# Kernel optimization log

Hardware: AMD Instinct MI355X
Metric: run time of the kernel (lower is better)

## Reference

```python
import jax, jax.numpy as jnp
import numpy as np

B, S, L, C = 256, 3, 4096, 2        # batch, num_slices, slice_length, in_channels
NN, CH, GH, HEADS = 4, 64, 64, 4    # num_nodes, cnn_hidden, gat_hidden, gat_heads
BD = CH * NN // 2                   # CNN branch_dim = 128
TD, TH, TL = 256, 4, 2              # transformer dim / heads / layers
NC = 5
DH = TD // TH


def setup_inputs():
    ks = iter(jax.random.split(jax.random.key(0), 128))
    def rn(shape, s=0.05):
        return jax.random.normal(next(ks), shape, jnp.float32) * s
    def bn(c):  # eval-mode BN params: gamma, beta, running_mean, running_var
        return (jax.random.uniform(next(ks), (2, c)) + 0.5, rn((2, c)),
                rn((2, c)), jax.random.uniform(next(ks), (2, c)) + 0.5)
    inp = {}
    inp['x_t'] = jax.random.normal(next(ks), (B, S, L, C), jnp.float32)
    inp['x_f'] = jax.random.uniform(next(ks), (B, S, L, C), jnp.float32)
    # dual-branch CNN params stacked on leading axis: [0]=time branch, [1]=freq branch
    inp['conv1_w'] = rn((2, 32, C, 15)); inp['conv1_b'] = rn((2, 32))
    inp['bn1_g'], inp['bn1_b'], inp['bn1_m'], inp['bn1_v'] = bn(32)
    inp['conv2_w'] = rn((2, 64, 32, 7)); inp['conv2_b'] = rn((2, 64))
    inp['bn2_g'], inp['bn2_b'], inp['bn2_m'], inp['bn2_v'] = bn(64)
    inp['conv3_w'] = rn((2, BD, 64, 3)); inp['conv3_b'] = rn((2, BD))
    inp['bn3_g'], inp['bn3_b'], inp['bn3_m'], inp['bn3_v'] = bn(BD)
    # PyG GATConv params (lin has no bias; att_src/att_dst per head; output bias)
    inp['gat_lin_w'] = rn((HEADS * GH, CH))
    inp['gat_att_src'] = rn((HEADS, GH)); inp['gat_att_dst'] = rn((HEADS, GH))
    inp['gat_bias'] = rn((HEADS * GH,))
    inp['feat_proj_w'] = rn((TD, NN * GH * HEADS)); inp['feat_proj_b'] = rn((TD,))
    # TransformerEncoder (post-norm, relu), params stacked over TL layers
    inp['tr_in_w'] = rn((TL, 3 * TD, TD)); inp['tr_in_b'] = rn((TL, 3 * TD))
    inp['tr_out_w'] = rn((TL, TD, TD)); inp['tr_out_b'] = rn((TL, TD))
    inp['tr_l1_w'] = rn((TL, 4 * TD, TD)); inp['tr_l1_b'] = rn((TL, 4 * TD))
    inp['tr_l2_w'] = rn((TL, TD, 4 * TD)); inp['tr_l2_b'] = rn((TL, TD))
    inp['tr_ln1_g'] = jnp.ones((TL, TD)); inp['tr_ln1_b'] = jnp.zeros((TL, TD))
    inp['tr_ln2_g'] = jnp.ones((TL, TD)); inp['tr_ln2_b'] = jnp.zeros((TL, TD))
    inp['ta_w'] = rn((1, TD)); inp['ta_b'] = rn((1,))
    inp['fc1_w'] = rn((128, TD)); inp['fc1_b'] = rn((128,))
    inp['fc2_w'] = rn((64, 128)); inp['fc2_b'] = rn((64,))
    inp['fc3_w'] = rn((NC, 64)); inp['fc3_b'] = rn((NC,))
    src = [i for i in range(NN) for j in range(NN) if i != j]
    dst = [j for i in range(NN) for j in range(NN) if i != j]
    inp['edge_index'] = jnp.array([src, dst], jnp.int32)
    return inp


def _conv_bn_relu(x, w, b, g, be, m, v, stride, pad):
    y = jax.lax.conv_general_dilated(x, w, (stride,), [(pad, pad)],
                                     dimension_numbers=('NCH', 'OIH', 'NCH'))
    y = (y + b[None, :, None] - m[None, :, None]) * (g / jnp.sqrt(v + 1e-5))[None, :, None] + be[None, :, None]
    return jax.nn.relu(y)


def _branch(x, c1w, c1b, g1, b1, m1, v1, c2w, c2b, g2, b2, m2, v2, c3w, c3b, g3, b3, m3, v3):
    y = _conv_bn_relu(x, c1w, c1b, g1, b1, m1, v1, 2, 7)
    y = _conv_bn_relu(y, c2w, c2b, g2, b2, m2, v2, 2, 3)
    y = _conv_bn_relu(y, c3w, c3b, g3, b3, m3, v3, 1, 1)
    return y.mean(axis=-1)  # AdaptiveAvgPool1d(1)


def _ln(x, g, b):
    mu = x.mean(-1, keepdims=True)
    var = ((x - mu) ** 2).mean(-1, keepdims=True)
    return (x - mu) / jnp.sqrt(var + 1e-5) * g + b


def _model(edge_index, x_t, x_f, conv1_w, conv1_b, bn1_g, bn1_b, bn1_m, bn1_v,
           conv2_w, conv2_b, bn2_g, bn2_b, bn2_m, bn2_v,
           conv3_w, conv3_b, bn3_g, bn3_b, bn3_m, bn3_v,
           gat_lin_w, gat_att_src, gat_att_dst, gat_bias,
           feat_proj_w, feat_proj_b,
           tr_in_w, tr_in_b, tr_out_w, tr_out_b, tr_l1_w, tr_l1_b, tr_l2_w, tr_l2_b,
           tr_ln1_g, tr_ln1_b, tr_ln2_g, tr_ln2_b,
           ta_w, ta_b, fc1_w, fc1_b, fc2_w, fc2_b, fc3_w, fc3_b):
    G = B * S  # fold (batch, slice) -> one big conv/GAT batch (replaces the python loops)
    xt = x_t.transpose(0, 1, 3, 2).reshape(G, C, L)
    xf = x_f.transpose(0, 1, 3, 2).reshape(G, C, L)
    xs = jnp.stack([xt, xf])  # [2, G, C, L]
    pooled = jax.vmap(_branch)(xs, conv1_w, conv1_b, bn1_g, bn1_b, bn1_m, bn1_v,
                               conv2_w, conv2_b, bn2_g, bn2_b, bn2_m, bn2_v,
                               conv3_w, conv3_b, bn3_g, bn3_b, bn3_m, bn3_v)  # [2, G, BD]
    feat = jnp.concatenate([pooled[0], pooled[1]], axis=1).reshape(G, NN, CH)
    # GATConv (dense over the tiny 4-node graph; softmax over in-edges per dest node)
    h = jnp.einsum('gnc,oc->gno', feat, gat_lin_w).reshape(G, NN, HEADS, GH)
    a_src = jnp.einsum('gnhd,hd->gnh', h, gat_att_src)
    a_dst = jnp.einsum('gnhd,hd->gnh', h, gat_att_dst)
    scores = jax.nn.leaky_relu(a_dst[:, :, None, :] + a_src[:, None, :, :], 0.2)  # [G,i,j,H]
    adj = jnp.zeros((NN, NN), bool).at[edge_index[1], edge_index[0]].set(True)
    adj = adj.at[jnp.arange(NN), jnp.arange(NN)].set(True)  # PyG adds self-loops
    alpha = jax.nn.softmax(jnp.where(adj[None, :, :, None], scores, -1e9), axis=2)
    gat_out = jnp.einsum('gijh,gjhd->gihd', alpha, h).reshape(G, NN, HEADS * GH) + gat_bias
    sl = gat_out.reshape(B, S, NN * HEADS * GH) @ feat_proj_w.T + feat_proj_b  # [B,S,TD]
    # positional encoding
    pos = jnp.arange(S, dtype=jnp.float32)[:, None]
    div = jnp.exp(jnp.arange(0, TD, 2, dtype=jnp.float32) * (-np.log(10000.0) / TD))
    pe = jnp.zeros((S, TD)).at[:, 0::2].set(jnp.sin(pos * div)).at[:, 1::2].set(jnp.cos(pos * div))
    x = sl + pe[None]
    # TransformerEncoder, post-norm, relu FFN
    for l in range(TL):
        qkv = x @ tr_in_w[l].T + tr_in_b[l]
        q, k, v = jnp.split(qkv, 3, axis=-1)
        q = q.reshape(B, S, TH, DH).transpose(0, 2, 1, 3)
        k = k.reshape(B, S, TH, DH).transpose(0, 2, 1, 3)
        v = v.reshape(B, S, TH, DH).transpose(0, 2, 1, 3)
        attn = jax.nn.softmax(jnp.einsum('bhqd,bhkd->bhqk', q, k) / np.sqrt(DH), axis=-1)
        a = jnp.einsum('bhqk,bhkd->bhqd', attn, v).transpose(0, 2, 1, 3).reshape(B, S, TD)
        a = a @ tr_out_w[l].T + tr_out_b[l]
        x = _ln(x + a, tr_ln1_g[l], tr_ln1_b[l])
        f = jax.nn.relu(x @ tr_l1_w[l].T + tr_l1_b[l]) @ tr_l2_w[l].T + tr_l2_b[l]
        x = _ln(x + f, tr_ln2_g[l], tr_ln2_b[l])
    w = jax.nn.softmax((x @ ta_w.T + ta_b)[..., 0], axis=1)  # [B,S] temporal attention
    ctx = jnp.einsum('bs,bsd->bd', w, x)
    o = jax.nn.relu(ctx @ fc1_w.T + fc1_b)
    o = jax.nn.relu(o @ fc2_w.T + fc2_b)
    return o @ fc3_w.T + fc3_b  # logits [B, NC]


def reference(x_t, x_f, conv1_w, conv1_b, bn1_g, bn1_b, bn1_m, bn1_v, conv2_w, conv2_b, bn2_g, bn2_b, bn2_m, bn2_v, conv3_w, conv3_b, bn3_g, bn3_b, bn3_m, bn3_v, gat_lin_w, gat_att_src, gat_att_dst, gat_bias, feat_proj_w, feat_proj_b, tr_in_w, tr_in_b, tr_out_w, tr_out_b, tr_l1_w, tr_l1_b, tr_l2_w, tr_l2_b, tr_ln1_g, tr_ln1_b, tr_ln2_g, tr_ln2_b, ta_w, ta_b, fc1_w, fc1_b, fc2_w, fc2_b, fc3_w, fc3_b, edge_index):
    return _model(edge_index, x_t, x_f, conv1_w, conv1_b, bn1_g, bn1_b, bn1_m, bn1_v,
                  conv2_w, conv2_b, bn2_g, bn2_b, bn2_m, bn2_v,
                  conv3_w, conv3_b, bn3_g, bn3_b, bn3_m, bn3_v,
                  gat_lin_w, gat_att_src, gat_att_dst, gat_bias,
                  feat_proj_w, feat_proj_b,
                  tr_in_w, tr_in_b, tr_out_w, tr_out_b, tr_l1_w, tr_l1_b, tr_l2_w, tr_l2_b,
                  tr_ln1_g, tr_ln1_b, tr_ln2_g, tr_ln2_b,
                  ta_w, ta_b, fc1_w, fc1_b, fc2_w, fc2_b, fc3_w, fc3_b)
```

## Files before the change

### kernel.cpp

```cpp
#include <hip/hip_runtime.h>
#include <math.h>

#define Bn 256
#define Sn 3
#define Ln 4096
#define Gn 768
#define TDn 256
#define TLn 2

#define WS_W1K   0
#define WS_W2K   1024
#define WS_W3K   15360
#define WS_H1    39936
#define WS_H2    40000
#define WS_H3    40128
#define WS_FPWH  40960
#define WS_INWH  172032
#define WS_OUTWH 368640
#define WS_L1WH  434176
#define WS_L2WH  696320
#define WS_POOL  958464
#define WS_XH    958464
#define WS_ABH   1056768
#define WS_SCR   1155072
#define WS_Y     1548288
#define WS_X     1744896

typedef _Float16 f16x8 __attribute__((ext_vector_type(8)));
typedef float f32x4 __attribute__((ext_vector_type(4)));
#define MFMA16(a,b,c) __builtin_amdgcn_mfma_f32_16x16x32_f16(a,b,c,0,0,0)

__global__ __launch_bounds__(256) void prep_kernel(
    const float* __restrict__ w1, const float* __restrict__ w2, const float* __restrict__ w3,
    const float* __restrict__ c1b, const float* __restrict__ g1, const float* __restrict__ b1,
    const float* __restrict__ m1, const float* __restrict__ v1,
    const float* __restrict__ c2b, const float* __restrict__ g2, const float* __restrict__ b2,
    const float* __restrict__ m2, const float* __restrict__ v2,
    const float* __restrict__ c3b, const float* __restrict__ g3, const float* __restrict__ b3,
    const float* __restrict__ m3, const float* __restrict__ v3,
    float* __restrict__ ws)
{
    int i = blockIdx.x * 256 + threadIdx.x;
    _Float16* w1k = (_Float16*)(ws + WS_W1K);
    _Float16* w2k = (_Float16*)(ws + WS_W2K);
    _Float16* w3k = (_Float16*)(ws + WS_W3K);
    if (i < 2048) {
        int k = i & 31, oc = (i >> 5) & 31, br = i >> 10;
        int c = k >> 4, tau = k & 15;
        int a = br * 32 + oc;
        float s = g1[a] / sqrtf(v1[a] + 1e-5f);
        float v = (tau < 15) ? w1[(((size_t)a * 2 + c) * 15) + tau] * s : 0.f;
        w1k[i] = (_Float16)v;
    }
    if (i < 28672) {
        int k = i % 224; int a = i / 224;
        int tblk = k >> 5, ic = k & 31;
        int t = (tblk < 4) ? 2 * tblk : 2 * (tblk - 4) + 1;
        float s = g2[a] / sqrtf(v2[a] + 1e-5f);
        w2k[i] = (_Float16)(w2[((size_t)a * 32 + ic) * 7 + t] * s);
    }
    if (i < 49152) {
        int k = i % 192; int a = i / 192;
        int t = k >> 6, ic = k & 63;
        float s = g3[a] / sqrtf(v3[a] + 1e-5f);
        w3k[i] = (_Float16)(w3[((size_t)a * 64 + ic) * 3 + t] * s);
    }
    if (i < 64)  { float s = g1[i] / sqrtf(v1[i] + 1e-5f); ws[WS_H1 + i] = (c1b[i] - m1[i]) * s + b1[i]; }
    if (i < 128) { float s = g2[i] / sqrtf(v2[i] + 1e-5f); ws[WS_H2 + i] = (c2b[i] - m2[i]) * s + b2[i]; }
    if (i < 256) { float s = g3[i] / sqrtf(v3[i] + 1e-5f); ws[WS_H3 + i] = (c3b[i] - m3[i]) * s + b3[i]; }
}

__global__ __launch_bounds__(256) void prep_tr_kernel(
    const float* __restrict__ fpw, const float* __restrict__ inw,
    const float* __restrict__ outw, const float* __restrict__ l1w,
    const float* __restrict__ l2w, float* __restrict__ ws)
{
    int i = blockIdx.x * 256 + threadIdx.x;
    _Float16* fpwh = (_Float16*)(ws + WS_FPWH);
    _Float16* inwh = (_Float16*)(ws + WS_INWH);
    _Float16* outwh = (_Float16*)(ws + WS_OUTWH);
    _Float16* l1wh = (_Float16*)(ws + WS_L1WH);
    _Float16* l2wh = (_Float16*)(ws + WS_L2WH);
    if (i < 262144) fpwh[i] = (_Float16)fpw[i];
    if (i < 393216) inwh[i] = (_Float16)inw[i];
    if (i < 131072) outwh[i] = (_Float16)outw[i];
    if (i < 524288) { l1wh[i] = (_Float16)l1w[i]; l2wh[i] = (_Float16)l2w[i]; }
}

__global__ __launch_bounds__(256, 3) void conv_mfma_kernel(
    const float* __restrict__ x_t, const float* __restrict__ x_f,
    const float* __restrict__ ws, float* __restrict__ pooled)
{
    __shared__ _Float16 xsf[2 * 576];
    __shared__ _Float16 y1[2][132 * 32];
    __shared__ _Float16 y2s[128 * 64];
    __shared__ float h1s[32];
    __shared__ float h2s[64];
    __shared__ float h3s[128];
    __shared__ float pbuf[128];

    const int g = blockIdx.x, br = blockIdx.y;
    const int tid = threadIdx.x;
    const int lane = tid & 63, wv = tid >> 6;
    const int l15 = lane & 15, q4 = lane >> 4;

    const float* xin = (br == 0 ? x_t : x_f) + (size_t)g * (Ln * 2);
    const _Float16* w1k = (const _Float16*)(ws + WS_W1K) + br * 1024;
    const _Float16* w2k = (const _Float16*)(ws + WS_W2K) + br * 14336;
    const _Float16* w3k = (const _Float16*)(ws + WS_W3K) + br * 24576;

    if (tid < 32)  h1s[tid] = ws[WS_H1 + br * 32 + tid];
    if (tid < 64)  h2s[tid] = ws[WS_H2 + br * 64 + tid];
    if (tid < 128) { h3s[tid] = ws[WS_H3 + br * 128 + tid]; pbuf[tid] = 0.f; }

    f16x8 a1[2];
    #pragma unroll
    for (int mt = 0; mt < 2; ++mt)
        a1[mt] = *(const f16x8*)(w1k + (mt * 16 + l15) * 32 + q4 * 8);

    const int mg = wv & 1, ng = wv >> 1;

    const _Float16* w2row = w2k + (size_t)l15 * 224 + q4 * 8;
    const _Float16* w3row = w3k + (size_t)(mg * 64 + l15) * 192 + q4 * 8;

    float pool_[4][4];
    #pragma unroll
    for (int mt = 0; mt < 4; ++mt)
        #pragma unroll
        for (int r = 0; r < 4; ++r) pool_[mt][r] = 0.f;

    const f32x4 vzero = {0.f, 0.f, 0.f, 0.f};

    for (int l = tid; l < 576; l += 256) {
        int xl = -17 + l;
        float a = 0.f, b = 0.f;
        if (xl >= 0 && xl < Ln) { float2 v = *(const float2*)(xin + (size_t)xl * 2); a = v.x; b = v.y; }
        xsf[l] = (_Float16)a; xsf[576 + l] = (_Float16)b;
    }
    __syncthreads();

    #pragma unroll 1
    for (int tile = 0; tile < 9; ++tile) {
        const int P0 = tile * 126;
        const int Q0 = 2 * P0 - 5;

        const uint* xsu = (const uint*)xsf;
        #pragma unroll 1
        for (int nt = wv; nt < 17; nt += 4) {
            int j0 = nt * 16 + l15;
            union { f16x8 v; uint u[4]; } bf;
            int ubase = (q4 >> 1) * 288 + j0 + (q4 & 1) * 4;
            #pragma unroll
            for (int ii = 0; ii < 4; ++ii) bf.u[ii] = xsu[ubase + ii];
            f32x4 c1acc[2] = {vzero, vzero};
            c1acc[0] = MFMA16(a1[0], bf.v, c1acc[0]);
            c1acc[1] = MFMA16(a1[1], bf.v, c1acc[1]);

            if (j0 <= 260) {
                int q = Q0 + j0;
                bool val = (q >= 0) && (q < 2048);
                int i = j0 >> 1, par = j0 & 1;
                #pragma unroll
                for (int mt = 0; mt < 2; ++mt) {
                    int oc0 = mt * 16 + q4 * 4;
                    union { _Float16 h[4]; uint2 u; } pk;
                    #pragma unroll
                    for (int r = 0; r < 4; ++r) {
                        float y = c1acc[mt][r] + h1s[oc0 + r];
                        y = y > 0.f ? y : 0.f;
                        pk.h[r] = val ? (_Float16)y : (_Float16)0.f;
                    }
                    int gq = mt * 2 + (q4 >> 1), sub = q4 & 1;
                    *(uint2*)(&y1[par][(i * 4 + (gq ^ (i & 3))) * 8 + sub * 4]) = pk.u;
                }
            }
        }
        __syncthreads();

        float2 xr0 = {0.f, 0.f}, xr1 = {0.f, 0.f}, xr2 = {0.f, 0.f};
        if (tile < 8) {
            const int xn0 = 4 * (P0 + 126) - 17;
            { int xl = xn0 + tid;       if (xl < Ln) xr0 = *(const float2*)(xin + (size_t)xl * 2); }
            { int xl = xn0 + tid + 256; if (xl < Ln) xr1 = *(const float2*)(xin + (size_t)xl * 2); }
            if (tid < 64) { int xl = xn0 + tid + 512; if (xl < Ln) xr2 = *(const float2*)(xin + (size_t)xl * 2); }
        }

        #pragma unroll 1
        for (int jj = 0; jj < 2; ++jj) {
            f32x4 c2[4] = {vzero, vzero, vzero, vzero};
            f16x8 a2c[4];
            #pragma unroll
            for (int mt = 0; mt < 4; ++mt)
                a2c[mt] = *(const f16x8*)(w2row + (size_t)mt * 16 * 224);
            const int n = wv * 32 + jj * 16 + l15;
            #pragma unroll 1
            for (int ks = 0; ks < 7; ++ks) {
                int roff = (ks < 4) ? ks : ks - 4;
                const _Float16* yb = y1[(ks < 4) ? 0 : 1];
                int i = n + roff;
                f16x8 bb = *(const f16x8*)(yb + (i * 4 + (q4 ^ (i & 3))) * 8);
                f16x8 a2n[4];
                if (ks < 6) {
                    #pragma unroll
                    for (int mt = 0; mt < 4; ++mt)
                        a2n[mt] = *(const f16x8*)(w2row + (size_t)mt * 16 * 224 + (ks + 1) * 32);
                }
                #pragma unroll
                for (int mt = 0; mt < 4; ++mt)
                    c2[mt] = MFMA16(a2c[mt], bb, c2[mt]);
                if (ks < 6) {
                    #pragma unroll
                    for (int mt = 0; mt < 4; ++mt) a2c[mt] = a2n[mt];
                }
            }
            int p2 = P0 - 1 + n;
            bool val = (p2 >= 0) && (p2 < 1024);
            #pragma unroll
            for (int mt = 0; mt < 4; ++mt) {
                int oc0 = mt * 16 + q4 * 4;
                union { _Float16 h[4]; uint2 u; } pk;
                #pragma unroll
                for (int r = 0; r < 4; ++r) {
                    float y = c2[mt][r] + h2s[oc0 + r];
                    y = y > 0.f ? y : 0.f;
                    pk.h[r] = val ? (_Float16)y : (_Float16)0.f;
                }
                int gq = oc0 >> 3, sub = q4 & 1;
                *(uint2*)(&y2s[(n * 8 + (gq ^ (n & 7))) * 8 + sub * 4]) = pk.u;
            }
        }

        if (tile < 8) {
            { int l = tid;       xsf[l] = (_Float16)xr0.x; xsf[576 + l] = (_Float16)xr0.y; }
            { int l = tid + 256; xsf[l] = (_Float16)xr1.x; xsf[576 + l] = (_Float16)xr1.y; }
            if (tid < 64) { int l = tid + 512; xsf[l] = (_Float16)xr2.x; xsf[576 + l] = (_Float16)xr2.y; }
        }
        __syncthreads();

        #pragma unroll 1
        for (int half = 0; half < 2; ++half) {
            f32x4 c3[4][2];
            #pragma unroll
            for (int mt = 0; mt < 4; ++mt) { c3[mt][0] = vzero; c3[mt][1] = vzero; }
            f16x8 a3c[4];
            #pragma unroll
            for (int mt = 0; mt < 4; ++mt)
                a3c[mt] = *(const f16x8*)(w3row + (size_t)mt * 16 * 192);
            #pragma unroll 1
            for (int ks = 0; ks < 6; ++ks) {
                int t = ks >> 1, ich = ks & 1;
                f16x8 b3[2];
                #pragma unroll
                for (int jj = 0; jj < 2; ++jj) {
                    int np = ng * 64 + (half * 2 + jj) * 16 + l15;
                    int r = np + t; r = r < 128 ? r : 127;
                    int gq3 = ich * 4 + q4;
                    b3[jj] = *(const f16x8*)(&y2s[(r * 8 + (gq3 ^ (r & 7))) * 8]);
                }
                f16x8 a3n[4];
                if (ks < 5) {
                    #pragma unroll
                    for (int mt = 0; mt < 4; ++mt)
                        a3n[mt] = *(const f16x8*)(w3row + (size_t)mt * 16 * 192 + (ks + 1) * 32);
                }
                #pragma unroll
                for (int mt = 0; mt < 4; ++mt) {
                    c3[mt][0] = MFMA16(a3c[mt], b3[0], c3[mt][0]);
                    c3[mt][1] = MFMA16(a3c[mt], b3[1], c3[mt][1]);
                }
                if (ks < 5) {
                    #pragma unroll
                    for (int mt = 0; mt < 4; ++mt) a3c[mt] = a3n[mt];
                }
            }
            #pragma unroll
            for (int mt = 0; mt < 4; ++mt) {
                int oc0 = mg * 64 + mt * 16 + q4 * 4;
                #pragma unroll
                for (int jj = 0; jj < 2; ++jj) {
                    int np = ng * 64 + (half * 2 + jj) * 16 + l15;
                    int p3 = P0 + np;
                    float valf = ((np < 126) && (p3 < 1024)) ? 1.f : 0.f;
                    #pragma unroll
                    for (int r = 0; r < 4; ++r) {
                        float y = c3[mt][jj][r] + h3s[oc0 + r];
                        y = y > 0.f ? y : 0.f;
                        pool_[mt][r] = fmaf(y, valf, pool_[mt][r]);
                    }
                }
            }
        }
    }

    #pragma unroll
    for (int mt = 0; mt < 4; ++mt)
        #pragma unroll
        for (int r = 0; r < 4; ++r) {
            float v = pool_[mt][r];
            v += __shfl_xor(v, 1, 64);
            v += __shfl_xor(v, 2, 64);
            v += __shfl_xor(v, 4, 64);
            v += __shfl_xor(v, 8, 64);
            if (l15 == 0) atomicAdd(&pbuf[mg * 64 + mt * 16 + q4 * 4 + r], v);
        }
    __syncthreads();
    if (tid < 128) pooled[g * 256 + br * 128 + tid] = pbuf[tid] * (1.f / 1024.f);
}

__global__ __launch_bounds__(256) void gat_kernel(
    const float* __restrict__ glw, const float* __restrict__ att_src,
    const float* __restrict__ att_dst, const float* __restrict__ gbias,
    const float* __restrict__ pooled, _Float16* __restrict__ gouth)
{
    __shared__ float feats[256];
    __shared__ float hs[4 * 256];
    __shared__ float av[32];
    __shared__ float alpha[64];

    int g = blockIdx.x, tid = threadIdx.x;
    feats[tid] = pooled[g * 256 + tid];
    __syncthreads();

    {
        int o = tid;
        const float* w = glw + o * 64;
        float a0 = 0, a1 = 0, a2 = 0, a3 = 0;
        for (int c = 0; c < 64; ++c) {
            float wvv = w[c];
            a0 = fmaf(feats[c],       wvv, a0);
            a1 = fmaf(feats[64 + c],  wvv, a1);
            a2 = fmaf(feats[128 + c], wvv, a2);
            a3 = fmaf(feats[192 + c], wvv, a3);
        }
        hs[o] = a0; hs[256 + o] = a1; hs[512 + o] = a2; hs[768 + o] = a3;
    }
    __syncthreads();

    if (tid < 32) {
        int n = (tid & 15) >> 2, hd = tid & 3;
        const float* aw = (tid < 16) ? att_src : att_dst;
        float s = 0;
        for (int d = 0; d < 64; ++d) s = fmaf(hs[n * 256 + hd * 64 + d], aw[hd * 64 + d], s);
        av[tid] = s;
    }
    __syncthreads();

    if (tid < 16) {
        int i = tid >> 2, hd = tid & 3;
        float sc[4], mx = -1e30f;
        #pragma unroll
        for (int j = 0; j < 4; ++j) {
            float v = av[16 + i * 4 + hd] + av[j * 4 + hd];
            v = v > 0.f ? v : 0.2f * v;
            sc[j] = v; mx = fmaxf(mx, v);
        }
        float den = 0;
        #pragma unroll
        for (int j = 0; j < 4; ++j) { sc[j] = expf(sc[j] - mx); den += sc[j]; }
        #pragma unroll
        for (int j = 0; j < 4; ++j) alpha[(i * 4 + j) * 4 + hd] = sc[j] / den;
    }
    __syncthreads();

    {
        int o = tid, hd = o >> 6;
        #pragma unroll
        for (int i = 0; i < 4; ++i) {
            float acc = gbias[o];
            #pragma unroll
            for (int j = 0; j < 4; ++j) acc = fmaf(alpha[(i * 4 + j) * 4 + hd], hs[j * 256 + o], acc);
            gouth[(size_t)g * 1024 + i * 256 + o] = (_Float16)acc;
        }
    }
}

template <int K, int MODE>
__global__ __launch_bounds__(256) void mfma_gemm_kernel(
    const _Float16* __restrict__ A, const _Float16* __restrict__ W,
    const float* __restrict__ bias, float* __restrict__ out32,
    _Float16* __restrict__ out16, int N)
{
    const int tid = threadIdx.x;
    const int wv = tid >> 6, l15 = tid & 15, q4 = (tid & 63) >> 4;
    const int m0 = blockIdx.x * 64 + wv * 16;
    const int n0 = blockIdx.y * 64;

    const f32x4 vzero = {0.f, 0.f, 0.f, 0.f};
    f32x4 acc[4] = {vzero, vzero, vzero, vzero};

    const _Float16* arow = A + (size_t)(m0 + l15) * K + q4 * 8;
    #pragma unroll 4
    for (int ks = 0; ks < K / 32; ++ks) {
        f16x8 a = *(const f16x8*)(arow + ks * 32);
        #pragma unroll
        for (int nt = 0; nt < 4; ++nt) {
            f16x8 b = *(const f16x8*)(W + (size_t)(n0 + nt * 16 + l15) * K + ks * 32 + q4 * 8);
            acc[nt] = MFMA16(a, b, acc[nt]);
        }
    }

    #pragma unroll
    for (int nt = 0; nt < 4; ++nt) {
        int n = n0 + nt * 16 + l15;
        float bs = bias[n];
        #pragma unroll
        for (int r = 0; r < 4; ++r) {
            int m = m0 + q4 * 4 + r;
            float v = acc[nt][r] + bs;
            if (MODE == 1) v = fmaxf(v, 0.f);
            if (MODE == 3) {
                int s = m % 3;
                int kk = n >> 1;
                float dv = expf((float)kk * -0.07195588f);
                float arg = (float)s * dv;
                v += (n & 1) ? cosf(arg) : sinf(arg);
            }
            if (MODE == 0 || MODE == 3) out32[(size_t)m * N + n] = v;
            if (MODE == 1 || MODE == 3) out16[(size_t)m * N + n] = (_Float16)v;
        }
    }
}

template <int K>
__global__ __launch_bounds__(256) void gemm_ln_kernel(
    const _Float16* __restrict__ A, const _Float16* __restrict__ W,
    const float* __restrict__ bias,
    const float* __restrict__ gamma, const float* __restrict__ beta,
    float* __restrict__ X, _Float16* __restrict__ XH)
{
    __shared__ float ys[16][260];
    const int tid = threadIdx.x;
    const int wv = tid >> 6, l15 = tid & 15, q4 = (tid & 63) >> 4;
    const int r0 = blockIdx.x * 16;
    const int n0 = wv * 64;

    const f32x4 vzero = {0.f, 0.f, 0.f, 0.f};
    f32x4 acc[4] = {vzero, vzero, vzero, vzero};

    const _Float16* arow = A + (size_t)(r0 + l15) * K + q4 * 8;
    #pragma unroll 4
    for (int ks = 0; ks < K / 32; ++ks) {
        f16x8 a = *(const f16x8*)(arow + ks * 32);
        #pragma unroll
        for (int nt = 0; nt < 4; ++nt) {
            f16x8 b = *(const f16x8*)(W + (size_t)(n0 + nt * 16 + l15) * K + ks * 32 + q4 * 8);
            acc[nt] = MFMA16(a, b, acc[nt]);
        }
    }

    #pragma unroll
    for (int nt = 0; nt < 4; ++nt) {
        int col = n0 + nt * 16 + l15;
        float bs = bias[col];
        #pragma unroll
        for (int r = 0; r < 4; ++r) {
            int rowl = q4 * 4 + r;
            ys[rowl][col] = acc[nt][r] + bs + X[(size_t)(r0 + rowl) * 256 + col];
        }
    }
    __syncthreads();

    {
        int row = tid >> 4, l16 = tid & 15;
        float s = 0, s2 = 0;
        #pragma unroll
        for (int c0 = 0; c0 < 256; c0 += 16) {
            float v = ys[row][c0 + l16]; s += v; s2 += v * v;
        }
        s += __shfl_xor(s, 1, 64);  s2 += __shfl_xor(s2, 1, 64);
        s += __shfl_xor(s, 2, 64);  s2 += __shfl_xor(s2, 2, 64);
        s += __shfl_xor(s, 4, 64);  s2 += __shfl_xor(s2, 4, 64);
        s += __shfl_xor(s, 8, 64);  s2 += __shfl_xor(s2, 8, 64);
        float mu = s * (1.f / 256.f);
        float var = s2 * (1.f / 256.f) - mu * mu;
        float inv = 1.0f / sqrtf(var + 1e-5f);
        #pragma unroll
        for (int c0 = 0; c0 < 256; c0 += 16) {
            int c = c0 + l16;
            float v = (ys[row][c] - mu) * inv * gamma[c] + beta[c];
            X[(size_t)(r0 + row) * 256 + c] = v;
            XH[(size_t)(r0 + row) * 256 + c] = (_Float16)v;
        }
    }
}

__global__ __launch_bounds__(256) void attn_kernel(
    const float* __restrict__ qkv, _Float16* __restrict__ abufh)
{
    int b = blockIdx.x, tid = threadIdx.x, head = tid >> 6, d = tid & 63;
    const float* base = qkv + (size_t)b * 3 * 768 + head * 64 + d;
    float q[3], k[3], v[3];
    #pragma unroll
    for (int s = 0; s < 3; ++s) {
        const float* row = base + s * 768;
        q[s] = row[0]; k[s] = row[256]; v[s] = row[512];
    }
    float sc[3][3];
    #pragma unroll
    for (int si = 0; si < 3; ++si)
        #pragma unroll
        for (int sj = 0; sj < 3; ++sj) {
            float p = q[si] * k[sj];
            #pragma unroll
            for (int m = 32; m > 0; m >>= 1) p += __shfl_xor(p, m, 64);
            sc[si][sj] = p * 0.125f;
        }
    #pragma unroll
    for (int si = 0; si < 3; ++si) {
        float mx = fmaxf(sc[si][0], fmaxf(sc[si][1], sc[si][2]));
        float e0 = expf(sc[si][0] - mx), e1 = expf(sc[si][1] - mx), e2 = expf(sc[si][2] - mx);
        float den = e0 + e1 + e2;
        float o = (e0 * v[0] + e1 * v[1] + e2 * v[2]) / den;
        abufh[(size_t)(b * 3 + si) * 256 + head * 64 + d] = (_Float16)o;
    }
}

__global__ __launch_bounds__(256) void head_kernel(
    const float* __restrict__ X, const float* __restrict__ taw, const float* __restrict__ tab,
    const float* __restrict__ f1w, const float* __restrict__ f1b,
    const float* __restrict__ f2w, const float* __restrict__ f2b,
    const float* __restrict__ f3w, const float* __restrict__ f3b,
    float* __restrict__ out)
{
    __shared__ float xs[3 * 256];
    __shared__ float wsm[3];
    __shared__ float cs[256];
    __shared__ float a1[128];
    __shared__ float a2[64];
    int b = blockIdx.x, tid = threadIdx.x;
    for (int idx = tid; idx < 768; idx += 256) xs[idx] = X[(size_t)b * 768 + idx];
    __syncthreads();
    if (tid < 3) {
        float s = tab[0];
        for (int d = 0; d < 256; ++d) s = fmaf(xs[tid * 256 + d], taw[d], s);
        wsm[tid] = s;
    }
    __syncthreads();
    {
        float m = fmaxf(wsm[0], fmaxf(wsm[1], wsm[2]));
        float e0 = expf(wsm[0] - m), e1 = expf(wsm[1] - m), e2 = expf(wsm[2] - m);
        float den = e0 + e1 + e2;
        cs[tid] = (e0 * xs[tid] + e1 * xs[256 + tid] + e2 * xs[512 + tid]) / den;
    }
    __syncthreads();
    if (tid < 128) {
        float a = f1b[tid];
        const float* w = f1w + tid * 256;
        for (int c = 0; c < 256; ++c) a = fmaf(cs[c], w[c], a);
        a1[tid] = fmaxf(a, 0.f);
    }
    __syncthreads();
    if (tid < 64) {
        float a = f2b[tid];
        const float* w = f2w + tid * 128;
        for (int c = 0; c < 128; ++c) a = fmaf(a1[c], w[c], a);
        a2[tid] = fmaxf(a, 0.f);
    }
    __syncthreads();
    if (tid < 5) {
        float a = f3b[tid];
        const float* w = f3w + tid * 64;
        for (int c = 0; c < 64; ++c) a = fmaf(a2[c], w[c], a);
        out[b * 5 + tid] = a;
    }
}

extern "C" void kernel_launch(void* const* d_in, const int* in_sizes, int n_in,
                              void* d_out, int out_size, void* d_ws, size_t ws_size,
                              hipStream_t stream) {
    const float* x_t     = (const float*)d_in[0];
    const float* x_f     = (const float*)d_in[1];
    const float* conv1_w = (const float*)d_in[2];
    const float* conv1_b = (const float*)d_in[3];
    const float* bn1_g   = (const float*)d_in[4];
    const float* bn1_b   = (const float*)d_in[5];
    const float* bn1_m   = (const float*)d_in[6];
    const float* bn1_v   = (const float*)d_in[7];
    const float* conv2_w = (const float*)d_in[8];
    const float* conv2_b = (const float*)d_in[9];
    const float* bn2_g   = (const float*)d_in[10];
    const float* bn2_b   = (const float*)d_in[11];
    const float* bn2_m   = (const float*)d_in[12];
    const float* bn2_v   = (const float*)d_in[13];
    const float* conv3_w = (const float*)d_in[14];
    const float* conv3_b = (const float*)d_in[15];
    const float* bn3_g   = (const float*)d_in[16];
    const float* bn3_b   = (const float*)d_in[17];
    const float* bn3_m   = (const float*)d_in[18];
    const float* bn3_v   = (const float*)d_in[19];
    const float* gat_lin_w   = (const float*)d_in[20];
    const float* gat_att_src = (const float*)d_in[21];
    const float* gat_att_dst = (const float*)d_in[22];
    const float* gat_bias    = (const float*)d_in[23];
    const float* feat_proj_w = (const float*)d_in[24];
    const float* feat_proj_b = (const float*)d_in[25];
    const float* tr_in_w  = (const float*)d_in[26];
    const float* tr_in_b  = (const float*)d_in[27];
    const float* tr_out_w = (const float*)d_in[28];
    const float* tr_out_b = (const float*)d_in[29];
    const float* tr_l1_w  = (const float*)d_in[30];
    const float* tr_l1_b  = (const float*)d_in[31];
    const float* tr_l2_w  = (const float*)d_in[32];
    const float* tr_l2_b  = (const float*)d_in[33];
    const float* tr_ln1_g = (const float*)d_in[34];
    const float* tr_ln1_b = (const float*)d_in[35];
    const float* tr_ln2_g = (const float*)d_in[36];
    const float* tr_ln2_b = (const float*)d_in[37];
    const float* ta_w  = (const float*)d_in[38];
    const float* ta_b  = (const float*)d_in[39];
    const float* fc1_w = (const float*)d_in[40];
    const float* fc1_b = (const float*)d_in[41];
    const float* fc2_w = (const float*)d_in[42];
    const float* fc2_b = (const float*)d_in[43];
    const float* fc3_w = (const float*)d_in[44];
    const float* fc3_b = (const float*)d_in[45];

    float* ws    = (float*)d_ws;
    float* POOL  = ws + WS_POOL;
    float* X     = ws + WS_X;
    float* QKV   = ws + WS_SCR;
    _Float16* GOUTH = (_Float16*)(ws + WS_SCR);
    _Float16* MIDH  = (_Float16*)(ws + WS_SCR);
    _Float16* XH    = (_Float16*)(ws + WS_XH);
    _Float16* ABH   = (_Float16*)(ws + WS_ABH);
    const _Float16* FPWH  = (const _Float16*)(ws + WS_FPWH);
    const _Float16* INWH  = (const _Float16*)(ws + WS_INWH);
    const _Float16* OUTWH = (const _Float16*)(ws + WS_OUTWH);
    const _Float16* L1WH  = (const _Float16*)(ws + WS_L1WH);
    const _Float16* L2WH  = (const _Float16*)(ws + WS_L2WH);
    float* out = (float*)d_out;

    prep_kernel<<<192, 256, 0, stream>>>(conv1_w, conv2_w, conv3_w,
        conv1_b, bn1_g, bn1_b, bn1_m, bn1_v,
        conv2_b, bn2_g, bn2_b, bn2_m, bn2_v,
        conv3_b, bn3_g, bn3_b, bn3_m, bn3_v, ws);
    prep_tr_kernel<<<2048, 256, 0, stream>>>(feat_proj_w, tr_in_w, tr_out_w,
                                             tr_l1_w, tr_l2_w, ws);

    conv_mfma_kernel<<<dim3(Gn, 2), 256, 0, stream>>>(x_t, x_f, ws, POOL);

    gat_kernel<<<Gn, 256, 0, stream>>>(gat_lin_w, gat_att_src, gat_att_dst, gat_bias,
                                       POOL, GOUTH);

    mfma_gemm_kernel<1024, 3><<<dim3(12, 4), 256, 0, stream>>>(
        GOUTH, FPWH, feat_proj_b, X, XH, 256);

    for (int l = 0; l < TLn; ++l) {
        mfma_gemm_kernel<256, 0><<<dim3(12, 12), 256, 0, stream>>>(
            XH, INWH + (size_t)l * 196608, tr_in_b + l * 768, QKV, nullptr, 768);
        attn_kernel<<<Bn, 256, 0, stream>>>(QKV, ABH);
        gemm_ln_kernel<256><<<48, 256, 0, stream>>>(
            ABH, OUTWH + (size_t)l * 65536, tr_out_b + l * 256,
            tr_ln1_g + l * 256, tr_ln1_b + l * 256, X, XH);
        mfma_gemm_kernel<256, 1><<<dim3(12, 16), 256, 0, stream>>>(
            XH, L1WH + (size_t)l * 262144, tr_l1_b + l * 1024, nullptr, MIDH, 1024);
        gemm_ln_kernel<1024><<<48, 256, 0, stream>>>(
            MIDH, L2WH + (size_t)l * 262144, tr_l2_b + l * 256,
            tr_ln2_g + l * 256, tr_ln2_b + l * 256, X, XH);
    }

    head_kernel<<<Bn, 256, 0, stream>>>(X, ta_w, ta_b, fc1_w, fc1_b,
                                        fc2_w, fc2_b, fc3_w, fc3_b, out);
}
```

Before: 764.8 us.

## Fuse transformer layer into attention and FFN kernels; restructure conv2 MFMA loop

The per-layer chain of QKV GEMM, attention, out-proj+LN, FFN1 and FFN2+LN, five launches, becomes two fused kernels. One kernel per batch computes QKV, attention, out-projection and LayerNorm in shared memory. The other runs FFN1 and FFN2 with LayerNorm over 16-row tiles, keeping the intermediate in LDS. This removes launch overhead and global round-trips of the QKV and MLP intermediates. The attention kernel uses only 3 of 16 MFMA rows, wasting matrix throughput, and the FFN kernel launches only 48 blocks. Separately, the conv2 stage now computes both column halves per weight load, and conv occupancy is lowered from 3 to 2 to make room for the extra registers.

```diff
diff --git a/kernel.cpp b/kernel.cpp
--- a/kernel.cpp
+++ b/kernel.cpp
@@ -21,9 +21,7 @@
 #define WS_L2WH  696320
 #define WS_POOL  958464
 #define WS_XH    958464
-#define WS_ABH   1056768
 #define WS_SCR   1155072
-#define WS_Y     1548288
 #define WS_X     1744896
 
 typedef _Float16 f16x8 __attribute__((ext_vector_type(8)));
@@ -87,7 +85,7 @@
     if (i < 524288) { l1wh[i] = (_Float16)l1w[i]; l2wh[i] = (_Float16)l2w[i]; }
 }
 
-__global__ __launch_bounds__(256, 3) void conv_mfma_kernel(
+__global__ __launch_bounds__(256, 2) void conv_mfma_kernel(
     const float* __restrict__ x_t, const float* __restrict__ x_f,
     const float* __restrict__ ws, float* __restrict__ pooled)
 {
@@ -185,20 +183,25 @@
             if (tid < 64) { int xl = xn0 + tid + 512; if (xl < Ln) xr2 = *(const float2*)(xin + (size_t)xl * 2); }
         }
 
-        #pragma unroll 1
-        for (int jj = 0; jj < 2; ++jj) {
-            f32x4 c2[4] = {vzero, vzero, vzero, vzero};
+        {
+            f32x4 c2[4][2];
+            #pragma unroll
+            for (int mt = 0; mt < 4; ++mt) { c2[mt][0] = vzero; c2[mt][1] = vzero; }
             f16x8 a2c[4];
             #pragma unroll
             for (int mt = 0; mt < 4; ++mt)
                 a2c[mt] = *(const f16x8*)(w2row + (size_t)mt * 16 * 224);
-            const int n = wv * 32 + jj * 16 + l15;
             #pragma unroll 1
             for (int ks = 0; ks < 7; ++ks) {
                 int roff = (ks < 4) ? ks : ks - 4;
                 const _Float16* yb = y1[(ks < 4) ? 0 : 1];
-                int i = n + roff;
-                f16x8 bb = *(const f16x8*)(yb + (i * 4 + (q4 ^ (i & 3))) * 8);
+                f16x8 bb[2];
+                #pragma unroll
+                for (int jj = 0; jj < 2; ++jj) {
+                    int n = wv * 32 + jj * 16 + l15;
+                    int i = n + roff;
+                    bb[jj] = *(const f16x8*)(yb + (i * 4 + (q4 ^ (i & 3))) * 8);
+                }
                 f16x8 a2n[4];
                 if (ks < 6) {
                     #pragma unroll
@@ -206,27 +209,33 @@
                         a2n[mt] = *(const f16x8*)(w2row + (size_t)mt * 16 * 224 + (ks + 1) * 32);
                 }
                 #pragma unroll
-                for (int mt = 0; mt < 4; ++mt)
-                    c2[mt] = MFMA16(a2c[mt], bb, c2[mt]);
+                for (int mt = 0; mt < 4; ++mt) {
+                    c2[mt][0] = MFMA16(a2c[mt], bb[0], c2[mt][0]);
+                    c2[mt][1] = MFMA16(a2c[mt], bb[1], c2[mt][1]);
+                }
                 if (ks < 6) {
                     #pragma unroll
                     for (int mt = 0; mt < 4; ++mt) a2c[mt] = a2n[mt];
                 }
             }
-            int p2 = P0 - 1 + n;
-            bool val = (p2 >= 0) && (p2 < 1024);
-            #pragma unroll
-            for (int mt = 0; mt < 4; ++mt) {
-                int oc0 = mt * 16 + q4 * 4;
-                union { _Float16 h[4]; uint2 u; } pk;
-                #pragma unroll
-                for (int r = 0; r < 4; ++r) {
-                    float y = c2[mt][r] + h2s[oc0 + r];
-                    y = y > 0.f ? y : 0.f;
-                    pk.h[r] = val ? (_Float16)y : (_Float16)0.f;
-                }
-                int gq = oc0 >> 3, sub = q4 & 1;
-                *(uint2*)(&y2s[(n * 8 + (gq ^ (n & 7))) * 8 + sub * 4]) = pk.u;
+            #pragma unroll
+            for (int jj = 0; jj < 2; ++jj) {
+                int n = wv * 32 + jj * 16 + l15;
+                int p2 = P0 - 1 + n;
+                bool val = (p2 >= 0) && (p2 < 1024);
+                #pragma unroll
+                for (int mt = 0; mt < 4; ++mt) {
+                    int oc0 = mt * 16 + q4 * 4;
+                    union { _Float16 h[4]; uint2 u; } pk;
+                    #pragma unroll
+                    for (int r = 0; r < 4; ++r) {
+                        float y = c2[mt][jj][r] + h2s[oc0 + r];
+                        y = y > 0.f ? y : 0.f;
+                        pk.h[r] = val ? (_Float16)y : (_Float16)0.f;
+                    }
+                    int gq = oc0 >> 3, sub = q4 & 1;
+                    *(uint2*)(&y2s[(n * 8 + (gq ^ (n & 7))) * 8 + sub * 4]) = pk.u;
+                }
             }
         }
 
@@ -374,16 +383,16 @@
     }
 }
 
-template <int K, int MODE>
-__global__ __launch_bounds__(256) void mfma_gemm_kernel(
+__global__ __launch_bounds__(256) void fproj_gemm_kernel(
     const _Float16* __restrict__ A, const _Float16* __restrict__ W,
     const float* __restrict__ bias, float* __restrict__ out32,
-    _Float16* __restrict__ out16, int N)
+    _Float16* __restrict__ out16)
 {
     const int tid = threadIdx.x;
     const int wv = tid >> 6, l15 = tid & 15, q4 = (tid & 63) >> 4;
     const int m0 = blockIdx.x * 64 + wv * 16;
     const int n0 = blockIdx.y * 64;
+    constexpr int K = 1024;
 
     const f32x4 vzero = {0.f, 0.f, 0.f, 0.f};
     f32x4 acc[4] = {vzero, vzero, vzero, vzero};
@@ -403,66 +412,206 @@
     for (int nt = 0; nt < 4; ++nt) {
         int n = n0 + nt * 16 + l15;
         float bs = bias[n];
+        int kk = n >> 1;
+        float dv = expf((float)kk * -0.07195588f);
         #pragma unroll
         for (int r = 0; r < 4; ++r) {
             int m = m0 + q4 * 4 + r;
             float v = acc[nt][r] + bs;
-            if (MODE == 1) v = fmaxf(v, 0.f);
-            if (MODE == 3) {
-                int s = m % 3;
-                int kk = n >> 1;
-                float dv = expf((float)kk * -0.07195588f);
-                float arg = (float)s * dv;
-                v += (n & 1) ? cosf(arg) : sinf(arg);
-            }
-            if (MODE == 0 || MODE == 3) out32[(size_t)m * N + n] = v;
-            if (MODE == 1 || MODE == 3) out16[(size_t)m * N + n] = (_Float16)v;
-        }
-    }
-}
-
-template <int K>
-__global__ __launch_bounds__(256) void gemm_ln_kernel(
-    const _Float16* __restrict__ A, const _Float16* __restrict__ W,
-    const float* __restrict__ bias,
-    const float* __restrict__ gamma, const float* __restrict__ beta,
-    float* __restrict__ X, _Float16* __restrict__ XH)
+            float arg = (float)(m % 3) * dv;
+            v += (n & 1) ? cosf(arg) : sinf(arg);
+            out32[(size_t)m * 256 + n] = v;
+            out16[(size_t)m * 256 + n] = (_Float16)v;
+        }
+    }
+}
+
+__global__ __launch_bounds__(256) void attn_fused_kernel(
+    _Float16* __restrict__ XH, float* __restrict__ X,
+    const _Float16* __restrict__ inw, const float* __restrict__ inb,
+    const _Float16* __restrict__ outw, const float* __restrict__ outb,
+    const float* __restrict__ gamma, const float* __restrict__ beta)
 {
+    __shared__ _Float16 xls[3 * 264];
+    __shared__ float qkvl[3 * 768];
+    __shared__ _Float16 aout[3 * 264];
+    __shared__ float ys[3][256];
+
+    const int b = blockIdx.x, tid = threadIdx.x;
+    const int wv = tid >> 6, lane = tid & 63;
+    const int l15 = tid & 15, q4 = (tid & 63) >> 4;
+    const int ml = (l15 < 3) ? l15 : 2;
+
+    for (int idx = tid; idx < 768; idx += 256)
+        xls[(idx >> 8) * 264 + (idx & 255)] = XH[(size_t)b * 768 + idx];
+    __syncthreads();
+
+    {
+        const int n0w = wv * 192;
+        const _Float16* arow = xls + ml * 264 + q4 * 8;
+        #pragma unroll 1
+        for (int nt = 0; nt < 12; ++nt) {
+            int col = n0w + nt * 16 + l15;
+            f32x4 acc = {0.f, 0.f, 0.f, 0.f};
+            #pragma unroll
+            for (int ks = 0; ks < 8; ++ks) {
+                f16x8 a = *(const f16x8*)(arow + ks * 32);
+                f16x8 bf = *(const f16x8*)(inw + (size_t)col * 256 + ks * 32 + q4 * 8);
+                acc = MFMA16(a, bf, acc);
+            }
+            if (q4 == 0) {
+                float bsv = inb[col];
+                #pragma unroll
+                for (int r = 0; r < 3; ++r)
+                    qkvl[r * 768 + col] = acc[r] + bsv;
+            }
+        }
+    }
+    __syncthreads();
+
+    {
+        const int hb = wv * 64 + lane;
+        float q[3], k[3], v[3];
+        #pragma unroll
+        for (int s = 0; s < 3; ++s) {
+            q[s] = qkvl[s * 768 + hb];
+            k[s] = qkvl[s * 768 + 256 + hb];
+            v[s] = qkvl[s * 768 + 512 + hb];
+        }
+        float sc[3][3];
+        #pragma unroll
+        for (int si = 0; si < 3; ++si)
+            #pragma unroll
+            for (int sj = 0; sj < 3; ++sj) {
+                float p = q[si] * k[sj];
+                #pragma unroll
+                for (int m = 32; m > 0; m >>= 1) p += __shfl_xor(p, m, 64);
+                sc[si][sj] = p * 0.125f;
+            }
+        #pragma unroll
+        for (int si = 0; si < 3; ++si) {
+            float mx = fmaxf(sc[si][0], fmaxf(sc[si][1], sc[si][2]));
+            float e0 = expf(sc[si][0] - mx), e1 = expf(sc[si][1] - mx), e2 = expf(sc[si][2] - mx);
+            float den = e0 + e1 + e2;
+            float o = (e0 * v[0] + e1 * v[1] + e2 * v[2]) / den;
+            aout[si * 264 + hb] = (_Float16)o;
+        }
+    }
+    __syncthreads();
+
+    {
+        const int n0w = wv * 64;
+        const _Float16* arow = aout + ml * 264 + q4 * 8;
+        #pragma unroll 1
+        for (int nt = 0; nt < 4; ++nt) {
+            int col = n0w + nt * 16 + l15;
+            f32x4 acc = {0.f, 0.f, 0.f, 0.f};
+            #pragma unroll
+            for (int ks = 0; ks < 8; ++ks) {
+                f16x8 a = *(const f16x8*)(arow + ks * 32);
+                f16x8 bf = *(const f16x8*)(outw + (size_t)col * 256 + ks * 32 + q4 * 8);
+                acc = MFMA16(a, bf, acc);
+            }
+            if (q4 == 0) {
+                float bsv = outb[col];
+                #pragma unroll
+                for (int r = 0; r < 3; ++r)
+                    ys[r][col] = acc[r] + bsv + X[((size_t)b * 3 + r) * 256 + col];
+            }
+        }
+    }
+    __syncthreads();
+
+    if (wv < 3) {
+        float s = 0.f, s2 = 0.f;
+        #pragma unroll
+        for (int c0 = 0; c0 < 256; c0 += 64) {
+            float v = ys[wv][c0 + lane]; s += v; s2 += v * v;
+        }
+        #pragma unroll
+        for (int m = 32; m > 0; m >>= 1) { s += __shfl_xor(s, m, 64); s2 += __shfl_xor(s2, m, 64); }
+        float mu = s * (1.f / 256.f);
+        float var = s2 * (1.f / 256.f) - mu * mu;
+        float inv = 1.f / sqrtf(var + 1e-5f);
+        #pragma unroll
+        for (int c0 = 0; c0 < 256; c0 += 64) {
+            int c = c0 + lane;
+            float v = (ys[wv][c] - mu) * inv * gamma[c] + beta[c];
+            X[((size_t)b * 3 + wv) * 256 + c] = v;
+            XH[((size_t)b * 3 + wv) * 256 + c] = (_Float16)v;
+        }
+    }
+}
+
+__global__ __launch_bounds__(256) void ffn_fused_kernel(
+    _Float16* __restrict__ XH, float* __restrict__ X,
+    const _Float16* __restrict__ l1w, const float* __restrict__ l1b,
+    const _Float16* __restrict__ l2w, const float* __restrict__ l2b,
+    const float* __restrict__ gamma, const float* __restrict__ beta)
+{
+    __shared__ _Float16 xls[16 * 264];
+    __shared__ _Float16 mid[16 * 1032];
     __shared__ float ys[16][260];
+
     const int tid = threadIdx.x;
     const int wv = tid >> 6, l15 = tid & 15, q4 = (tid & 63) >> 4;
     const int r0 = blockIdx.x * 16;
-    const int n0 = wv * 64;
-
-    const f32x4 vzero = {0.f, 0.f, 0.f, 0.f};
-    f32x4 acc[4] = {vzero, vzero, vzero, vzero};
-
-    const _Float16* arow = A + (size_t)(r0 + l15) * K + q4 * 8;
-    #pragma unroll 4
-    for (int ks = 0; ks < K / 32; ++ks) {
-        f16x8 a = *(const f16x8*)(arow + ks * 32);
+
+    for (int idx = tid; idx < 4096; idx += 256)
+        xls[(idx >> 8) * 264 + (idx & 255)] = XH[(size_t)r0 * 256 + idx];
+    __syncthreads();
+
+    {
+        const _Float16* arow = xls + l15 * 264 + q4 * 8;
+        #pragma unroll 1
+        for (int nt = 0; nt < 16; ++nt) {
+            int col = wv * 256 + nt * 16 + l15;
+            f32x4 acc = {0.f, 0.f, 0.f, 0.f};
+            #pragma unroll
+            for (int ks = 0; ks < 8; ++ks) {
+                f16x8 a = *(const f16x8*)(arow + ks * 32);
+                f16x8 bf = *(const f16x8*)(l1w + (size_t)col * 256 + ks * 32 + q4 * 8);
+                acc = MFMA16(a, bf, acc);
+            }
+            float bsv = l1b[col];
+            #pragma unroll
+            for (int r = 0; r < 4; ++r) {
+                float v = fmaxf(acc[r] + bsv, 0.f);
+                mid[(q4 * 4 + r) * 1032 + col] = (_Float16)v;
+            }
+        }
+    }
+    __syncthreads();
+
+    {
+        const _Float16* arow = mid + l15 * 1032 + q4 * 8;
+        const f32x4 vzero = {0.f, 0.f, 0.f, 0.f};
+        f32x4 acc[4] = {vzero, vzero, vzero, vzero};
+        #pragma unroll 2
+        for (int ks = 0; ks < 32; ++ks) {
+            f16x8 a = *(const f16x8*)(arow + ks * 32);
+            #pragma unroll
+            for (int nt = 0; nt < 4; ++nt) {
+                f16x8 bf = *(const f16x8*)(l2w + (size_t)(wv * 64 + nt * 16 + l15) * 1024 + ks * 32 + q4 * 8);
+                acc[nt] = MFMA16(a, bf, acc[nt]);
+            }
+        }
         #pragma unroll
         for (int nt = 0; nt < 4; ++nt) {
-            f16x8 b = *(const f16x8*)(W + (size_t)(n0 + nt * 16 + l15) * K + ks * 32 + q4 * 8);
-            acc[nt] = MFMA16(a, b, acc[nt]);
-        }
-    }
-
-    #pragma unroll
-    for (int nt = 0; nt < 4; ++nt) {
-        int col = n0 + nt * 16 + l15;
-        float bs = bias[col];
-        #pragma unroll
-        for (int r = 0; r < 4; ++r) {
-            int rowl = q4 * 4 + r;
-            ys[rowl][col] = acc[nt][r] + bs + X[(size_t)(r0 + rowl) * 256 + col];
+            int col = wv * 64 + nt * 16 + l15;
+            float bsv = l2b[col];
+            #pragma unroll
+            for (int r = 0; r < 4; ++r) {
+                int row = q4 * 4 + r;
+                ys[row][col] = acc[nt][r] + bsv + X[(size_t)(r0 + row) * 256 + col];
+            }
         }
     }
     __syncthreads();
 
     {
         int row = tid >> 4, l16 = tid & 15;
-        float s = 0, s2 = 0;
+        float s = 0.f, s2 = 0.f;
         #pragma unroll
         for (int c0 = 0; c0 < 256; c0 += 16) {
             float v = ys[row][c0 + l16]; s += v; s2 += v * v;
@@ -481,37 +630,6 @@
             X[(size_t)(r0 + row) * 256 + c] = v;
             XH[(size_t)(r0 + row) * 256 + c] = (_Float16)v;
         }
-    }
-}
-
-__global__ __launch_bounds__(256) void attn_kernel(
-    const float* __restrict__ qkv, _Float16* __restrict__ abufh)
-{
-    int b = blockIdx.x, tid = threadIdx.x, head = tid >> 6, d = tid & 63;
-    const float* base = qkv + (size_t)b * 3 * 768 + head * 64 + d;
-    float q[3], k[3], v[3];
-    #pragma unroll
-    for (int s = 0; s < 3; ++s) {
-        const float* row = base + s * 768;
-        q[s] = row[0]; k[s] = row[256]; v[s] = row[512];
-    }
-    float sc[3][3];
-    #pragma unroll
-    for (int si = 0; si < 3; ++si)
-        #pragma unroll
-        for (int sj = 0; sj < 3; ++sj) {
-            float p = q[si] * k[sj];
-            #pragma unroll
-            for (int m = 32; m > 0; m >>= 1) p += __shfl_xor(p, m, 64);
-            sc[si][sj] = p * 0.125f;
-        }
-    #pragma unroll
-    for (int si = 0; si < 3; ++si) {
-        float mx = fmaxf(sc[si][0], fmaxf(sc[si][1], sc[si][2]));
-        float e0 = expf(sc[si][0] - mx), e1 = expf(sc[si][1] - mx), e2 = expf(sc[si][2] - mx);
-        float den = e0 + e1 + e2;
-        float o = (e0 * v[0] + e1 * v[1] + e2 * v[2]) / den;
-        abufh[(size_t)(b * 3 + si) * 256 + head * 64 + d] = (_Float16)o;
     }
 }
 
@@ -618,11 +736,8 @@
     float* ws    = (float*)d_ws;
     float* POOL  = ws + WS_POOL;
     float* X     = ws + WS_X;
-    float* QKV   = ws + WS_SCR;
     _Float16* GOUTH = (_Float16*)(ws + WS_SCR);
-    _Float16* MIDH  = (_Float16*)(ws + WS_SCR);
     _Float16* XH    = (_Float16*)(ws + WS_XH);
-    _Float16* ABH   = (_Float16*)(ws + WS_ABH);
     const _Float16* FPWH  = (const _Float16*)(ws + WS_FPWH);
     const _Float16* INWH  = (const _Float16*)(ws + WS_INWH);
     const _Float16* OUTWH = (const _Float16*)(ws + WS_OUTWH);
@@ -642,21 +757,18 @@
     gat_kernel<<<Gn, 256, 0, stream>>>(gat_lin_w, gat_att_src, gat_att_dst, gat_bias,
                                        POOL, GOUTH);
 
-    mfma_gemm_kernel<1024, 3><<<dim3(12, 4), 256, 0, stream>>>(
-        GOUTH, FPWH, feat_proj_b, X, XH, 256);
+    fproj_gemm_kernel<<<dim3(12, 4), 256, 0, stream>>>(
+        GOUTH, FPWH, feat_proj_b, X, XH);
 
     for (int l = 0; l < TLn; ++l) {
-        mfma_gemm_kernel<256, 0><<<dim3(12, 12), 256, 0, stream>>>(
-            XH, INWH + (size_t)l * 196608, tr_in_b + l * 768, QKV, nullptr, 768);
-        attn_kernel<<<Bn, 256, 0, stream>>>(QKV, ABH);
-        gemm_ln_kernel<256><<<48, 256, 0, stream>>>(
-            ABH, OUTWH + (size_t)l * 65536, tr_out_b + l * 256,
-            tr_ln1_g + l * 256, tr_ln1_b + l * 256, X, XH);
-        mfma_gemm_kernel<256, 1><<<dim3(12, 16), 256, 0, stream>>>(
-            XH, L1WH + (size_t)l * 262144, tr_l1_b + l * 1024, nullptr, MIDH, 1024);
-        gemm_ln_kernel<1024><<<48, 256, 0, stream>>>(
-            MIDH, L2WH + (size_t)l * 262144, tr_l2_b + l * 256,
-            tr_ln2_g + l * 256, tr_ln2_b + l * 256, X, XH);
+        attn_fused_kernel<<<Bn, 256, 0, stream>>>(
+            XH, X, INWH + (size_t)l * 196608, tr_in_b + l * 768,
+            OUTWH + (size_t)l * 65536, tr_out_b + l * 256,
+            tr_ln1_g + l * 256, tr_ln1_b + l * 256);
+        ffn_fused_kernel<<<Gn / 16, 256, 0, stream>>>(
+            XH, X, L1WH + (size_t)l * 262144, tr_l1_b + l * 1024,
+            L2WH + (size_t)l * 262144, tr_l2_b + l * 256,
+            tr_ln2_g + l * 256, tr_ln2_b + l * 256);
     }
 
     head_kernel<<<Bn, 256, 0, stream>>>(X, ta_w, ta_b, fc1_w, fc1_b,
```

Result: faster. 707.7 us (-7.5%).
